# Kernel tuning notes

Hardware: AMD Instinct MI355X
Metric: run time of the kernel (lower is better)

The kernel has to match this reference:

```python
import jax, jax.numpy as jnp
import numpy as np

G = 32            # gridsize
N = G * G         # num_nodes = 1024
F_IN = 32         # input_dim
H = 256           # hidden_dim
L = 4             # n_layers
B = 64            # batch
MID = F_IN + L * H
MIN_VAL = -10000000.0
EPS_LN = 1e-5
EPS_BN = 1e-5


def _grid_edges():
    ids = np.arange(N).reshape(G, G)
    hs, hd = ids[:, :-1].ravel(), ids[:, 1:].ravel()
    vs, vd = ids[:-1, :].ravel(), ids[1:, :].ravel()
    src = np.concatenate([hs, hd, vs, vd]).astype(np.int32)
    dst = np.concatenate([hd, hs, vd, vs]).astype(np.int32)
    return jnp.asarray(src), jnp.asarray(dst)


def setup_inputs() -> dict:
    key = jax.random.key(0)
    ks = jax.random.split(key, 16)
    mask_f = jax.random.bernoulli(ks[0], 0.7, (B, N)).astype(jnp.float32)
    feats = jax.random.normal(ks[1], (B, N * F_IN), dtype=jnp.float32)
    observations = jnp.concatenate([mask_f, feats], axis=1)
    src, dst = _grid_edges()
    def lin(k, fi, fo):
        return jax.random.normal(k, (fi, fo), dtype=jnp.float32) / np.sqrt(fi)
    W0 = lin(ks[2], F_IN, H); b0 = jnp.zeros((H,), jnp.float32)
    g0 = jnp.ones((H,), jnp.float32); be0 = jnp.zeros((H,), jnp.float32)
    Ws = jax.random.normal(ks[3], (L - 1, H, H), jnp.float32) / np.sqrt(H)
    bs = jnp.zeros((L - 1, H), jnp.float32)
    gs = jnp.ones((L - 1, H), jnp.float32); bes = jnp.zeros((L - 1, H), jnp.float32)
    W1 = lin(ks[4], MID, 2 * H); b1 = jnp.zeros((2 * H,), jnp.float32)
    bn_g = jnp.ones((2 * H,), jnp.float32); bn_b = jnp.zeros((2 * H,), jnp.float32)
    bn_m = jax.random.normal(ks[5], (2 * H,), jnp.float32) * 0.1
    bn_v = jax.random.uniform(ks[6], (2 * H,), jnp.float32, 0.5, 1.5)
    W2 = lin(ks[7], 2 * H, 1); b2 = jnp.zeros((1,), jnp.float32)
    return {"observations": observations, "src": src, "dst": dst,
            "W0": W0, "b0": b0, "g0": g0, "be0": be0,
            "Ws": Ws, "bs": bs, "gs": gs, "bes": bes,
            "W1": W1, "b1": b1, "bn_g": bn_g, "bn_b": bn_b,
            "bn_m": bn_m, "bn_v": bn_v, "W2": W2, "b2": b2}


def _layer_norm(z, g, b):
    mu = z.mean(-1, keepdims=True)
    var = z.var(-1, keepdims=True)
    return (z - mu) / jnp.sqrt(var + EPS_LN) * g + b


def reference(observations, src, dst, W0, b0, g0, be0, Ws, bs, gs, bes,
              W1, b1, bn_g, bn_b, bn_m, bn_v, W2, b2):
    mask = observations[:, :N] != 0.0                      # [B,N] bool action mask
    x = observations[:, N:].reshape(B, N, F_IN)            # node features
    outs = [x]
    h = x
    for l in range(L):
        # GIN with eps=-1: (1+eps)*x_i vanishes -> mlp(sum of neighbor features)
        agg = jnp.zeros_like(h).at[:, dst, :].add(h[:, src, :])
        W, bb, g, be = ((W0, b0, g0, be0) if l == 0
                        else (Ws[l - 1], bs[l - 1], gs[l - 1], bes[l - 1]))
        h = jax.nn.relu(_layer_norm(agg @ W + bb, g, be))  # mlp ReLU; outer .relu() is idempotent
        outs.append(h)
    xc = jnp.concatenate(outs, axis=-1).reshape(B * N, MID)
    z = xc @ W1 + b1
    z = (z - bn_m) / jnp.sqrt(bn_v + EPS_BN) * bn_g + bn_b  # BatchNorm1d eval mode
    z = jax.nn.relu(z)                                       # dropout off in eval
    y = (z @ W2 + b2).reshape(B, N)
    return jnp.where(mask, y, MIN_VAL)
```

## Files before the change

### kernel.cpp

```cpp
#include <hip/hip_runtime.h>
#include <stdint.h>

#define FIN 32
#define HD 256
#define MIDK 1056
#define HF 512
#define MROWS 65536
#define OBS_STRIDE 33792

typedef float f32x2 __attribute__((ext_vector_type(2)));
typedef float f32x4 __attribute__((ext_vector_type(4)));

__device__ __forceinline__ unsigned pack4fp8(float a, float b, float c, float d) {
    int w = __builtin_amdgcn_cvt_pk_fp8_f32(a, b, 0, false);
    return (unsigned)__builtin_amdgcn_cvt_pk_fp8_f32(c, d, w, true);
}
__device__ __forceinline__ unsigned char f2fp8(float f) {
    return (unsigned char)(__builtin_amdgcn_cvt_pk_fp8_f32(f, f, 0, false) & 0xff);
}

__device__ __forceinline__ void glds16(const void* g, void* l) {
    __builtin_amdgcn_global_load_lds(
        (const __attribute__((address_space(1))) unsigned int*)g,
        (__attribute__((address_space(3))) unsigned int*)l,
        16, 0, 0);
}

__device__ __forceinline__ void gather16(const float* __restrict__ src, int stride, int n,
                                         unsigned char* __restrict__ dst) {
    float f[16];
#pragma unroll
    for (int j = 0; j < 16; ++j) f[j] = src[(size_t)j * stride + n];
    uint4 o;
    o.x = pack4fp8(f[0],  f[1],  f[2],  f[3]);
    o.y = pack4fp8(f[4],  f[5],  f[6],  f[7]);
    o.z = pack4fp8(f[8],  f[9],  f[10], f[11]);
    o.w = pack4fp8(f[12], f[13], f[14], f[15]);
    *(uint4*)dst = o;
}

__global__ __launch_bounds__(256) void k_prep_w(
        const float* __restrict__ W0, const float* __restrict__ Ws,
        const float* __restrict__ W1,
        unsigned char* __restrict__ Wt0, unsigned char* __restrict__ WtL,
        unsigned char* __restrict__ WtF) {
    const int b = blockIdx.x, t = threadIdx.x;
    if (b < 2) {
        int s = b * 256 + t;
        int hh = s >> 8, n = s & 255;
        gather16(W0 + (size_t)(hh * 16) * HD, HD, n, Wt0 + (size_t)s * 16);
    } else if (b < 50) {
        int u = (b - 2) * 256 + t;
        int l = u >> 12, s = u & 4095;
        int kb = s >> 9, hh = (s >> 8) & 1, n = s & 255;
        gather16(Ws + (size_t)l * 65536 + (size_t)(kb * 32 + hh * 16) * HD, HD, n,
                 WtL + (size_t)l * 65536 + (size_t)s * 16);
    } else {
        int s = (b - 50) * 256 + t;
        int kb = s >> 11, hh = (s >> 9) & 3, n = s & 511;
        int k0 = kb * 64 + hh * 16;
        if (k0 < MIDK)
            gather16(W1 + (size_t)k0 * HF, HF, n, WtF + (size_t)s * 16);
        else
            *(uint4*)(WtF + (size_t)s * 16) = make_uint4(0, 0, 0, 0);
    }
}

template <int K>
__global__ __launch_bounds__(256, 4) void k_layer(
        const unsigned char* __restrict__ Hin,
        const float* __restrict__ obs,
        const unsigned char* __restrict__ Wt,
        const float* __restrict__ bias, const float* __restrict__ gamma,
        const float* __restrict__ beta, unsigned char* __restrict__ Hout) {
    constexpr int KB = K / 32;
    __shared__ __align__(16) unsigned char Agg[(K / 16) * 64 * 16];
    __shared__ float ls[64], lss[64];
    const int t = threadIdx.x;
    const int w = t >> 6, lane = t & 63, quad = lane >> 4, l15 = lane & 15;
    const int q1 = quad >> 1, q0 = quad & 1;
    const int m0 = ((blockIdx.x & 7) * 128 + (blockIdx.x >> 3)) * 64;
    if (t < 64) { ls[t] = 0.f; lss[t] = 0.f; }

    if constexpr (K == 256) {
        const int r32 = t >> 3, seg = t & 7;
        const size_t rowBase = (size_t)(m0 & ~1023);
#pragma unroll
        for (int p = 0; p < 2; ++p) {
            const int r = p * 32 + r32;
            const int node = (m0 + r) & 1023;
            const int rr = node >> 5, cc = node & 31;
            float s[32];
#pragma unroll
            for (int i = 0; i < 32; ++i) s[i] = 0.f;
            auto addn = [&](int nn) {
                const uint4* pp = (const uint4*)(Hin + (rowBase + nn) * (size_t)K + seg * 32);
                uint4 u0 = pp[0], u1 = pp[1];
                unsigned uu[8] = {u0.x, u0.y, u0.z, u0.w, u1.x, u1.y, u1.z, u1.w};
#pragma unroll
                for (int i = 0; i < 8; ++i) {
                    f32x2 lo = __builtin_amdgcn_cvt_pk_f32_fp8(uu[i], false);
                    f32x2 hi = __builtin_amdgcn_cvt_pk_f32_fp8(uu[i], true);
                    s[4 * i + 0] += lo.x; s[4 * i + 1] += lo.y;
                    s[4 * i + 2] += hi.x; s[4 * i + 3] += hi.y;
                }
            };
            if (cc > 0)  addn(node - 1);
            if (cc < 31) addn(node + 1);
            if (rr > 0)  addn(node - 32);
            if (rr < 31) addn(node + 32);
            unsigned ow[8];
#pragma unroll
            for (int i = 0; i < 8; ++i)
                ow[i] = pack4fp8(s[4 * i], s[4 * i + 1], s[4 * i + 2], s[4 * i + 3]);
            ((uint4*)Agg)[(2 * seg) * 64 + r]     = make_uint4(ow[0], ow[1], ow[2], ow[3]);
            ((uint4*)Agg)[(2 * seg + 1) * 64 + r] = make_uint4(ow[4], ow[5], ow[6], ow[7]);
        }
    } else {
        const int r = t >> 2, seg4 = t & 3;
        const int bimg = m0 >> 10;
        const int node = (m0 + r) & 1023;
        const int rr = node >> 5, cc = node & 31;
        const float* fb = obs + (size_t)bimg * OBS_STRIDE + 1024 + seg4 * 8;
        float s[8] = {0, 0, 0, 0, 0, 0, 0, 0};
        auto addnf = [&](int nn) {
            const float4* fp = (const float4*)(fb + nn * 32);
            float4 f0 = fp[0], f1 = fp[1];
            s[0] += f0.x; s[1] += f0.y; s[2] += f0.z; s[3] += f0.w;
            s[4] += f1.x; s[5] += f1.y; s[6] += f1.z; s[7] += f1.w;
        };
        if (cc > 0)  addnf(node - 1);
        if (cc < 31) addnf(node + 1);
        if (rr > 0)  addnf(node - 32);
        if (rr < 31) addnf(node + 32);
        uint2 o;
        o.x = pack4fp8(s[0], s[1], s[2], s[3]);
        o.y = pack4fp8(s[4], s[5], s[6], s[7]);
        *(uint2*)(Agg + ((seg4 >> 1) * 64 + r) * 16 + (seg4 & 1) * 8) = o;
    }
    __syncthreads();

    f32x4 acc[4][4] = {};
    const unsigned char* bbase = Wt + ((size_t)(q1 * 256 + w * 64 + l15)) * 16 + q0 * 8;
    const unsigned char* abase = Agg + ((size_t)(q1 * 64 + l15)) * 16 + q0 * 8;

#define LOADBL(dst, kb) { const unsigned char* bp = bbase + (size_t)(kb) * 8192; \
    dst[0] = *(const long long*)(bp);        dst[1] = *(const long long*)(bp + 256); \
    dst[2] = *(const long long*)(bp + 512);  dst[3] = *(const long long*)(bp + 768); }
#define MFMAL(buf, kb) { long long af[4]; \
    _Pragma("unroll") for (int mt = 0; mt < 4; ++mt) \
        af[mt] = *(const long long*)(abase + (kb) * 2048 + mt * 256); \
    _Pragma("unroll") for (int mt = 0; mt < 4; ++mt) \
    _Pragma("unroll") for (int nt = 0; nt < 4; ++nt) \
        acc[mt][nt] = __builtin_amdgcn_mfma_f32_16x16x32_fp8_fp8(af[mt], buf[nt], acc[mt][nt], 0, 0, 0); }

    if constexpr (KB == 1) {
        long long bA[4];
        LOADBL(bA, 0);
        MFMAL(bA, 0);
    } else {
        long long bA[4], bB[4];
        LOADBL(bA, 0);
#pragma unroll
        for (int j = 0; j < KB / 2 - 1; ++j) {
            LOADBL(bB, 2 * j + 1);
            MFMAL(bA, 2 * j);
            LOADBL(bA, 2 * j + 2);
            MFMAL(bB, 2 * j + 1);
        }
        LOADBL(bB, KB - 1);
        MFMAL(bA, KB - 2);
        MFMAL(bB, KB - 1);
    }
#undef LOADBL
#undef MFMAL

#pragma unroll
    for (int mt = 0; mt < 4; ++mt) {
        float s0 = 0, s1 = 0, s2 = 0, s3 = 0, u0 = 0, u1 = 0, u2 = 0, u3 = 0;
#pragma unroll
        for (int nt = 0; nt < 4; ++nt) {
            int col = w * 64 + nt * 16 + l15;
            float bv = bias[col];
            f32x4 vv = acc[mt][nt];
            vv.x += bv; vv.y += bv; vv.z += bv; vv.w += bv;
            acc[mt][nt] = vv;
            s0 += vv.x; u0 += vv.x * vv.x;
            s1 += vv.y; u1 += vv.y * vv.y;
            s2 += vv.z; u2 += vv.z * vv.z;
            s3 += vv.w; u3 += vv.w * vv.w;
        }
#pragma unroll
        for (int msk = 1; msk < 16; msk <<= 1) {
            s0 += __shfl_xor(s0, msk); u0 += __shfl_xor(u0, msk);
            s1 += __shfl_xor(s1, msk); u1 += __shfl_xor(u1, msk);
            s2 += __shfl_xor(s2, msk); u2 += __shfl_xor(u2, msk);
            s3 += __shfl_xor(s3, msk); u3 += __shfl_xor(u3, msk);
        }
        if (l15 == 0) {
            int rl = mt * 16 + quad * 4;
            atomicAdd(&ls[rl + 0], s0); atomicAdd(&lss[rl + 0], u0);
            atomicAdd(&ls[rl + 1], s1); atomicAdd(&lss[rl + 1], u1);
            atomicAdd(&ls[rl + 2], s2); atomicAdd(&lss[rl + 2], u2);
            atomicAdd(&ls[rl + 3], s3); atomicAdd(&lss[rl + 3], u3);
        }
    }
    __syncthreads();
#pragma unroll
    for (int mt = 0; mt < 4; ++mt) {
        int rl = mt * 16 + quad * 4;
        float mu0 = ls[rl + 0] * (1.f / 256.f), mu1 = ls[rl + 1] * (1.f / 256.f);
        float mu2 = ls[rl + 2] * (1.f / 256.f), mu3 = ls[rl + 3] * (1.f / 256.f);
        float rs0 = rsqrtf(lss[rl + 0] * (1.f / 256.f) - mu0 * mu0 + 1e-5f);
        float rs1 = rsqrtf(lss[rl + 1] * (1.f / 256.f) - mu1 * mu1 + 1e-5f);
        float rs2 = rsqrtf(lss[rl + 2] * (1.f / 256.f) - mu2 * mu2 + 1e-5f);
        float rs3 = rsqrtf(lss[rl + 3] * (1.f / 256.f) - mu3 * mu3 + 1e-5f);
#pragma unroll
        for (int nt = 0; nt < 4; ++nt) {
            int col = w * 64 + nt * 16 + l15;
            float gg = gamma[col], be = beta[col];
            f32x4 vv = acc[mt][nt];
            size_t rb = (size_t)(m0 + mt * 16 + quad * 4) * HD + col;
            Hout[rb]          = f2fp8(fmaxf((vv.x - mu0) * rs0 * gg + be, 0.f));
            Hout[rb + HD]     = f2fp8(fmaxf((vv.y - mu1) * rs1 * gg + be, 0.f));
            Hout[rb + 2 * HD] = f2fp8(fmaxf((vv.z - mu2) * rs2 * gg + be, 0.f));
            Hout[rb + 3 * HD] = f2fp8(fmaxf((vv.w - mu3) * rs3 * gg + be, 0.f));
        }
    }
}

__global__ __launch_bounds__(512, 6) void k_final(
        const unsigned char* __restrict__ h0, const unsigned char* __restrict__ h1,
        const unsigned char* __restrict__ h2, const unsigned char* __restrict__ h3,
        const unsigned char* __restrict__ WtF,
        const float* __restrict__ b1,
        const float* __restrict__ bng, const float* __restrict__ bnb,
        const float* __restrict__ bnm, const float* __restrict__ bnv,
        const float* __restrict__ W2, const float* __restrict__ b2,
        const float* __restrict__ obs, float* __restrict__ out) {
    __shared__ __align__(16) unsigned char As[32 * 67 * 16];
    __shared__ float yred[32];
    const int t = threadIdx.x;
    const int w = t >> 6, lane = t & 63, quad = lane >> 4, l15 = lane & 15;
    const int q1 = quad >> 1, q0 = quad & 1;
    const int m0 = ((blockIdx.x & 7) * 256 + (blockIdx.x >> 3)) * 32;
    const int bimg = m0 >> 10, node0 = m0 & 1023;
    if (t < 32) yred[t] = 0.f;

    const unsigned char* hbuf[4] = {h0, h1, h2, h3};
    {
        const unsigned char* hb = hbuf[lane >> 4];
        const int colo = (lane & 15) * 16;
#pragma unroll
        for (int i = 0; i < 4; ++i) {
            int r = i * 8 + w;
            glds16(hb + (size_t)(m0 + r) * HD + colo, As + (size_t)(r * 67 + 2) * 16);
        }
    }
    if (t < 64) {
        int hh = t & 1, r = t >> 1;
        const float* p = obs + (size_t)bimg * OBS_STRIDE + 1024 + (node0 + r) * 32 + hh * 16;
        float4 f0 = *(const float4*)p, f1 = *(const float4*)(p + 4);
        float4 f2 = *(const float4*)(p + 8), f3 = *(const float4*)(p + 12);
        uint4 o;
        o.x = pack4fp8(f0.x, f0.y, f0.z, f0.w);
        o.y = pack4fp8(f1.x, f1.y, f1.z, f1.w);
        o.z = pack4fp8(f2.x, f2.y, f2.z, f2.w);
        o.w = pack4fp8(f3.x, f3.y, f3.z, f3.w);
        *(uint4*)(As + (r * 67 + hh) * 16) = o;
    }
    __syncthreads();

    f32x4 acc[2][4] = {};
    const unsigned char* bbase = WtF + ((size_t)(q1 * 512 + w * 64 + l15)) * 16 + q0 * 8;
    const unsigned char* abase0 = As + ((size_t)((0 * 16 + l15) * 67 + q1)) * 16 + q0 * 8;
    const unsigned char* abase1 = As + ((size_t)((1 * 16 + l15) * 67 + q1)) * 16 + q0 * 8;

#define LOADBF(dst, c) { const unsigned char* bp = bbase + (size_t)(c) * 16384; \
    dst[0] = *(const long long*)(bp);        dst[1] = *(const long long*)(bp + 256); \
    dst[2] = *(const long long*)(bp + 512);  dst[3] = *(const long long*)(bp + 768); }
#define MFMAF(buf, c) { \
    long long a0 = *(const long long*)(abase0 + (c) * 32); \
    long long a1 = *(const long long*)(abase1 + (c) * 32); \
    _Pragma("unroll") for (int nt = 0; nt < 4; ++nt) { \
        acc[0][nt] = __builtin_amdgcn_mfma_f32_16x16x32_fp8_fp8(a0, buf[nt], acc[0][nt], 0, 0, 0); \
        acc[1][nt] = __builtin_amdgcn_mfma_f32_16x16x32_fp8_fp8(a1, buf[nt], acc[1][nt], 0, 0, 0); } }

    long long bA[4], bB[4];
    LOADBF(bA, 0);
#pragma unroll
    for (int cc = 0; cc < 16; ++cc) {
        LOADBF(bB, 2 * cc + 1);
        MFMAF(bA, 2 * cc);
        LOADBF(bA, 2 * cc + 2);
        MFMAF(bB, 2 * cc + 1);
    }
    MFMAF(bA, 32);
#undef LOADBF
#undef MFMAF

    float scv[4], sbv[4], w2v[4];
#pragma unroll
    for (int nt = 0; nt < 4; ++nt) {
        int col = w * 64 + nt * 16 + l15;
        float sc = bng[col] * rsqrtf(bnv[col] + 1e-5f);
        scv[nt] = sc;
        sbv[nt] = (b1[col] - bnm[col]) * sc + bnb[col];
        w2v[nt] = W2[col];
    }
#pragma unroll
    for (int mt = 0; mt < 2; ++mt) {
        float p0 = 0, p1 = 0, p2 = 0, p3 = 0;
#pragma unroll
        for (int nt = 0; nt < 4; ++nt) {
            f32x4 vv = acc[mt][nt];
            p0 += fmaxf(vv.x * scv[nt] + sbv[nt], 0.f) * w2v[nt];
            p1 += fmaxf(vv.y * scv[nt] + sbv[nt], 0.f) * w2v[nt];
            p2 += fmaxf(vv.z * scv[nt] + sbv[nt], 0.f) * w2v[nt];
            p3 += fmaxf(vv.w * scv[nt] + sbv[nt], 0.f) * w2v[nt];
        }
#pragma unroll
        for (int msk = 1; msk < 16; msk <<= 1) {
            p0 += __shfl_xor(p0, msk);
            p1 += __shfl_xor(p1, msk);
            p2 += __shfl_xor(p2, msk);
            p3 += __shfl_xor(p3, msk);
        }
        if (l15 == 0) {
            int rl = mt * 16 + quad * 4;
            atomicAdd(&yred[rl + 0], p0);
            atomicAdd(&yred[rl + 1], p1);
            atomicAdd(&yred[rl + 2], p2);
            atomicAdd(&yred[rl + 3], p3);
        }
    }
    __syncthreads();
    if (t < 32) {
        int gm = m0 + t;
        float mk = obs[(size_t)bimg * OBS_STRIDE + (node0 + t)];
        out[gm] = (mk != 0.f) ? yred[t] + b2[0] : -10000000.0f;
    }
}

extern "C" void kernel_launch(void* const* d_in, const int* in_sizes, int n_in,
                              void* d_out, int out_size, void* d_ws, size_t ws_size,
                              hipStream_t stream) {
    const float* obs = (const float*)d_in[0];
    const float* W0  = (const float*)d_in[3];
    const float* b0  = (const float*)d_in[4];
    const float* g0  = (const float*)d_in[5];
    const float* be0 = (const float*)d_in[6];
    const float* Ws  = (const float*)d_in[7];
    const float* bs  = (const float*)d_in[8];
    const float* gs  = (const float*)d_in[9];
    const float* bes = (const float*)d_in[10];
    const float* W1  = (const float*)d_in[11];
    const float* b1  = (const float*)d_in[12];
    const float* bng = (const float*)d_in[13];
    const float* bnb = (const float*)d_in[14];
    const float* bnm = (const float*)d_in[15];
    const float* bnv = (const float*)d_in[16];
    const float* W2  = (const float*)d_in[17];
    const float* b2  = (const float*)d_in[18];
    float* out = (float*)d_out;

    char* ws = (char*)d_ws;
    unsigned char* h0  = (unsigned char*)(ws);
    unsigned char* h1  = (unsigned char*)(ws + 16777216);
    unsigned char* h2  = (unsigned char*)(ws + 33554432);
    unsigned char* h3  = (unsigned char*)(ws + 50331648);
    unsigned char* Wt0 = (unsigned char*)(ws + 67108864);
    unsigned char* WtL = (unsigned char*)(ws + 67117056);
    unsigned char* WtF = (unsigned char*)(ws + 67313664);

    k_prep_w<<<182, 256, 0, stream>>>(W0, Ws, W1, Wt0, WtL, WtF);

    k_layer<FIN><<<1024, 256, 0, stream>>>(h0 , obs, Wt0, b0, g0, be0, h0);
    k_layer<HD> <<<1024, 256, 0, stream>>>(h0, obs, WtL,              bs,       gs,       bes,       h1);
    k_layer<HD> <<<1024, 256, 0, stream>>>(h1, obs, WtL + 65536,      bs + 256, gs + 256, bes + 256, h2);
    k_layer<HD> <<<1024, 256, 0, stream>>>(h2, obs, WtL + 2 * 65536,  bs + 512, gs + 512, bes + 512, h3);

    k_final<<<2048, 512, 0, stream>>>(h0, h1, h2, h3, WtF, b1, bng, bnb, bnm, bnv,
                                      W2, b2, obs, out);
}
```

Baseline: 243.8 us.

## Restructure final GEMM to 64-row tiles with LDS-staged weights over K loop

Result: no change. 242.3 us (-0.6%).

```diff
diff --git a/kernel.cpp b/kernel.cpp
--- a/kernel.cpp
+++ b/kernel.cpp
@@ -229,7 +229,7 @@
     }
 }
 
-__global__ __launch_bounds__(512, 6) void k_final(
+__global__ __launch_bounds__(512) void k_final(
         const unsigned char* __restrict__ h0, const unsigned char* __restrict__ h1,
         const unsigned char* __restrict__ h2, const unsigned char* __restrict__ h3,
         const unsigned char* __restrict__ WtF,
@@ -238,71 +238,72 @@
         const float* __restrict__ bnm, const float* __restrict__ bnv,
         const float* __restrict__ W2, const float* __restrict__ b2,
         const float* __restrict__ obs, float* __restrict__ out) {
-    __shared__ __align__(16) unsigned char As[32 * 67 * 16];
-    __shared__ float yred[32];
+    __shared__ __align__(16) unsigned char As[264 * 16];
+    __shared__ __align__(16) unsigned char Bsm[2056 * 16];
+    __shared__ float yred[64];
     const int t = threadIdx.x;
     const int w = t >> 6, lane = t & 63, quad = lane >> 4, l15 = lane & 15;
     const int q1 = quad >> 1, q0 = quad & 1;
-    const int m0 = ((blockIdx.x & 7) * 256 + (blockIdx.x >> 3)) * 32;
+    const int wr = w >> 2, wc = w & 3;
+    const int m0 = ((blockIdx.x & 7) * 128 + (blockIdx.x >> 3)) * 64;
     const int bimg = m0 >> 10, node0 = m0 & 1023;
-    if (t < 32) yred[t] = 0.f;
+    if (t < 64) yred[t] = 0.f;
 
     const unsigned char* hbuf[4] = {h0, h1, h2, h3};
-    {
-        const unsigned char* hb = hbuf[lane >> 4];
-        const int colo = (lane & 15) * 16;
-#pragma unroll
-        for (int i = 0; i < 4; ++i) {
-            int r = i * 8 + w;
-            glds16(hb + (size_t)(m0 + r) * HD + colo, As + (size_t)(r * 67 + 2) * 16);
-        }
-    }
-    if (t < 64) {
-        int hh = t & 1, r = t >> 1;
-        const float* p = obs + (size_t)bimg * OBS_STRIDE + 1024 + (node0 + r) * 32 + hh * 16;
-        float4 f0 = *(const float4*)p, f1 = *(const float4*)(p + 4);
-        float4 f2 = *(const float4*)(p + 8), f3 = *(const float4*)(p + 12);
-        uint4 o;
-        o.x = pack4fp8(f0.x, f0.y, f0.z, f0.w);
-        o.y = pack4fp8(f1.x, f1.y, f1.z, f1.w);
-        o.z = pack4fp8(f2.x, f2.y, f2.z, f2.w);
-        o.w = pack4fp8(f3.x, f3.y, f3.z, f3.w);
-        *(uint4*)(As + (r * 67 + hh) * 16) = o;
-    }
-    __syncthreads();
-
-    f32x4 acc[2][4] = {};
-    const unsigned char* bbase = WtF + ((size_t)(q1 * 512 + w * 64 + l15)) * 16 + q0 * 8;
-    const unsigned char* abase0 = As + ((size_t)((0 * 16 + l15) * 67 + q1)) * 16 + q0 * 8;
-    const unsigned char* abase1 = As + ((size_t)((1 * 16 + l15) * 67 + q1)) * 16 + q0 * 8;
-
-#define LOADBF(dst, c) { const unsigned char* bp = bbase + (size_t)(c) * 16384; \
-    dst[0] = *(const long long*)(bp);        dst[1] = *(const long long*)(bp + 256); \
-    dst[2] = *(const long long*)(bp + 512);  dst[3] = *(const long long*)(bp + 768); }
-#define MFMAF(buf, c) { \
-    long long a0 = *(const long long*)(abase0 + (c) * 32); \
-    long long a1 = *(const long long*)(abase1 + (c) * 32); \
-    _Pragma("unroll") for (int nt = 0; nt < 4; ++nt) { \
-        acc[0][nt] = __builtin_amdgcn_mfma_f32_16x16x32_fp8_fp8(a0, buf[nt], acc[0][nt], 0, 0, 0); \
-        acc[1][nt] = __builtin_amdgcn_mfma_f32_16x16x32_fp8_fp8(a1, buf[nt], acc[1][nt], 0, 0, 0); } }
-
-    long long bA[4], bB[4];
-    LOADBF(bA, 0);
-#pragma unroll
-    for (int cc = 0; cc < 16; ++cc) {
-        LOADBF(bB, 2 * cc + 1);
-        MFMAF(bA, 2 * cc);
-        LOADBF(bA, 2 * cc + 2);
-        MFMAF(bB, 2 * cc + 1);
-    }
-    MFMAF(bA, 32);
-#undef LOADBF
-#undef MFMAF
-
-    float scv[4], sbv[4], w2v[4];
-#pragma unroll
-    for (int nt = 0; nt < 4; ++nt) {
-        int col = w * 64 + nt * 16 + l15;
+    f32x4 acc[2][8] = {};
+
+    for (int iter = 0; iter < 17; ++iter) {
+        const int kb = iter * 64;
+        const int steps = (iter < 16) ? 2 : 1;
+        if (iter == 0) {
+            if (t < 128) {
+                int h = t >> 6, r = t & 63;
+                const float* p = obs + (size_t)bimg * OBS_STRIDE + 1024 + (node0 + r) * 32 + h * 16;
+                float4 f0 = *(const float4*)p, f1 = *(const float4*)(p + 4);
+                float4 f2 = *(const float4*)(p + 8), f3 = *(const float4*)(p + 12);
+                uint4 o;
+                o.x = pack4fp8(f0.x, f0.y, f0.z, f0.w);
+                o.y = pack4fp8(f1.x, f1.y, f1.z, f1.w);
+                o.z = pack4fp8(f2.x, f2.y, f2.z, f2.w);
+                o.w = pack4fp8(f3.x, f3.y, f3.z, f3.w);
+                *(uint4*)(As + (h * 66 + r) * 16) = o;
+            } else if (t < 256) {
+                int h = t >> 6;
+                glds16(h0 + (size_t)(m0 + (t & 63)) * HD + (h - 2) * 16,
+                       As + (size_t)h * 66 * 16);
+            }
+        } else if (t < steps * 128) {
+            int h = t >> 6, r = t & 63;
+            int j = kb + h * 16 - FIN;
+            glds16(hbuf[j >> 8] + (size_t)(m0 + r) * HD + (j & 255),
+                   As + (size_t)h * 66 * 16);
+        }
+        for (int i = 0; i < steps * 2; ++i)
+            glds16(WtF + ((size_t)iter * 2048 + i * 512 + t) * 16,
+                   Bsm + ((size_t)i * 514 + (t & ~63)) * 16);
+        __syncthreads();
+#pragma unroll 2
+        for (int s2 = 0; s2 < steps; ++s2) {
+            long long af[2], bf[8];
+#pragma unroll
+            for (int mt = 0; mt < 2; ++mt)
+                af[mt] = *(const long long*)(As + ((s2 * 2 + q1) * 66 + wr * 32 + mt * 16 + l15) * 16 + q0 * 8);
+#pragma unroll
+            for (int nt = 0; nt < 8; ++nt)
+                bf[nt] = *(const long long*)(Bsm + ((size_t)((s2 * 2 + q1) * 514 + wc * 128 + nt * 16 + l15)) * 16 + q0 * 8);
+#pragma unroll
+            for (int mt = 0; mt < 2; ++mt)
+#pragma unroll
+                for (int nt = 0; nt < 8; ++nt)
+                    acc[mt][nt] = __builtin_amdgcn_mfma_f32_16x16x32_fp8_fp8(af[mt], bf[nt], acc[mt][nt], 0, 0, 0);
+        }
+        __syncthreads();
+    }
+
+    float scv[8], sbv[8], w2v[8];
+#pragma unroll
+    for (int nt = 0; nt < 8; ++nt) {
+        int col = wc * 128 + nt * 16 + l15;
         float sc = bng[col] * rsqrtf(bnv[col] + 1e-5f);
         scv[nt] = sc;
         sbv[nt] = (b1[col] - bnm[col]) * sc + bnb[col];
@@ -312,7 +313,7 @@
     for (int mt = 0; mt < 2; ++mt) {
         float p0 = 0, p1 = 0, p2 = 0, p3 = 0;
 #pragma unroll
-        for (int nt = 0; nt < 4; ++nt) {
+        for (int nt = 0; nt < 8; ++nt) {
             f32x4 vv = acc[mt][nt];
             p0 += fmaxf(vv.x * scv[nt] + sbv[nt], 0.f) * w2v[nt];
             p1 += fmaxf(vv.y * scv[nt] + sbv[nt], 0.f) * w2v[nt];
@@ -327,7 +328,7 @@
             p3 += __shfl_xor(p3, msk);
         }
         if (l15 == 0) {
-            int rl = mt * 16 + quad * 4;
+            int rl = wr * 32 + mt * 16 + quad * 4;
             atomicAdd(&yred[rl + 0], p0);
             atomicAdd(&yred[rl + 1], p1);
             atomicAdd(&yred[rl + 2], p2);
@@ -335,7 +336,7 @@
         }
     }
     __syncthreads();
-    if (t < 32) {
+    if (t < 64) {
         int gm = m0 + t;
         float mk = obs[(size_t)bimg * OBS_STRIDE + (node0 + t)];
         out[gm] = (mk != 0.f) ? yred[t] + b2[0] : -10000000.0f;
@@ -380,6 +381,6 @@
     k_layer<HD> <<<1024, 256, 0, stream>>>(h1, obs, WtL + 65536,      bs + 256, gs + 256, bes + 256, h2);
     k_layer<HD> <<<1024, 256, 0, stream>>>(h2, obs, WtL + 2 * 65536,  bs + 512, gs + 512, bes + 512, h3);
 
-    k_final<<<2048, 512, 0, stream>>>(h0, h1, h2, h3, WtF, b1, bng, bnb, bnm, bnv,
+    k_final<<<1024, 512, 0, stream>>>(h0, h1, h2, h3, WtF, b1, bng, bnb, bnm, bnv,
                                       W2, b2, obs, out);
 }
```
